# Optimization experiments

Hardware: AMD Instinct MI355X
Metric: run time of the kernel (lower is better)

The kernel has to match this reference:

```python
import jax, jax.numpy as jnp
import numpy as np

VOCAB, EMB, HID = 32000, 512, 1024
B, T = 16, 128


def setup_inputs() -> dict:
    key = jax.random.key(0)
    ks = jax.random.split(key, 12)
    bound = 1.0 / np.sqrt(HID)
    u = lambda k, shape: jax.random.uniform(k, shape, jnp.float32, -bound, bound)
    return {
        "sentence": jax.random.randint(ks[0], (B, T), 0, VOCAB),
        "emb": jax.random.normal(ks[1], (VOCAB, EMB), jnp.float32),
        "W_i": u(ks[2], (EMB + HID, HID)), "b_i": u(ks[3], (HID,)),
        "W_f": u(ks[4], (EMB + HID, HID)), "b_f": u(ks[5], (HID,)),
        "W_o": u(ks[6], (EMB + HID, HID)), "b_o": u(ks[7], (HID,)),
        "W_c": u(ks[8], (EMB + HID, HID)), "b_c": u(ks[9], (HID,)),
        "W_hq": u(ks[10], (HID, VOCAB)), "b_q": u(ks[11], (VOCAB,)),
    }


def reference(sentence, emb, W_i, b_i, W_f, b_f, W_o, b_o, W_c, b_c, W_hq, b_q):
    # [B,T,E] -> [T,B,E]
    x = jnp.swapaxes(emb[sentence], 0, 1)
    # Fuse the 4 gate matmuls into one concatenated-weight matmul (same math).
    W = jnp.concatenate([W_i, W_f, W_o, W_c], axis=1)  # [E+H, 4H]
    b = jnp.concatenate([b_i, b_f, b_o, b_c])          # [4H]
    h0 = jnp.zeros((x.shape[1], HID), x.dtype)

    def step(carry, xt):
        h, c = carry
        z = jnp.concatenate([xt, h], axis=1) @ W + b   # [B,4H]
        i, f, o, g = jnp.split(z, 4, axis=1)
        i, f, o = jax.nn.sigmoid(i), jax.nn.sigmoid(f), jax.nn.sigmoid(o)
        c = f * c + i * jnp.tanh(g)
        h = o * jnp.tanh(c)
        return (h, c), h

    _, hs = jax.lax.scan(step, (h0, h0), x)            # [T,B,H]
    out = jnp.einsum('tbh,hv->tbv', hs, W_hq) + b_q    # [T,B,V]
    return jnp.transpose(out, (1, 2, 0))               # [B,V,T] as in torch permute(1,2,0)
```

## Files before the change

kernel.cpp:

```cpp
#include <hip/hip_runtime.h>
#include <math.h>

typedef float f32x4 __attribute__((ext_vector_type(4)));
typedef short bf16x8 __attribute__((ext_vector_type(8)));
typedef unsigned short u16;
typedef unsigned int u32;

#define FLAG_STRIDE 16
#define ACQ_BASE    8192
#define EPOCH_BASE  8448
#define QCNT_BASE   8512
#define FLAG_WORDS  ((QCNT_BASE + 16) * FLAG_STRIDE)
#define NTILE       125

__device__ __forceinline__ u16 f2bf(float f) {
    union { float f; unsigned u; } x; x.f = f;
    unsigned r = x.u + 0x7fff + ((x.u >> 16) & 1);
    return (u16)(r >> 16);
}

__device__ __forceinline__ void gload_lds16(const u16* g, u16* l) {
    __builtin_amdgcn_global_load_lds(
        (const __attribute__((address_space(1))) void*)g,
        (__attribute__((address_space(3))) void*)l, 16, 0, 0);
}

__global__ __launch_bounds__(256) void prep(
    const int* __restrict__ sent, const float* __restrict__ emb, u16* __restrict__ xb,
    const float* __restrict__ bi, const float* __restrict__ bf_,
    const float* __restrict__ bo, const float* __restrict__ bc, float* __restrict__ b4,
    const float* __restrict__ Wi, const float* __restrict__ Wf,
    const float* __restrict__ Wo, const float* __restrict__ Wc, u16* __restrict__ wxt,
    const float* __restrict__ Whq, u16* __restrict__ whqt) {
    __shared__ float tile[32][33];
    const int bx = blockIdx.x, tid = threadIdx.x;
    if (bx < 1024) {
        int row = bx * 2 + (tid >> 7);
        int t = row >> 4, b = row & 15;
        int idx = sent[b * 128 + t];
        float4 v = ((const float4*)(emb + (size_t)idx * 512))[tid & 127];
        ushort4 s = { f2bf(v.x), f2bf(v.y), f2bf(v.z), f2bf(v.w) };
        ((ushort4*)(xb + (size_t)row * 512))[tid & 127] = s;
        return;
    }
    if (bx < 1040) {
        int i = (bx - 1024) * 256 + tid;
        const float* p = (i < 1024) ? bi : (i < 2048) ? bf_ : (i < 3072) ? bo : bc;
        b4[i] = p[i & 1023];
        return;
    }
    const float* in; u16* out; int ldin, ldout, rt, ct;
    if (bx < 3088) {
        int q = bx - 1040, g = q >> 9, r = q & 511;
        in = (g == 0) ? Wi : (g == 1) ? Wf : (g == 2) ? Wo : Wc;
        ldin = 1024; out = wxt + (size_t)g * 1024 * 512; ldout = 512;
        rt = (r >> 5) * 32; ct = (r & 31) * 32;
    } else {
        int q = bx - 3088;
        in = Whq; ldin = 32000; out = whqt; ldout = 1024;
        rt = (q / 1000) * 32; ct = (q % 1000) * 32;
    }
    {
        int r = tid >> 3, cq = (tid & 7) * 4;
        float4 v = *(const float4*)(in + (size_t)(rt + r) * ldin + ct + cq);
        tile[r][cq] = v.x; tile[r][cq + 1] = v.y; tile[r][cq + 2] = v.z; tile[r][cq + 3] = v.w;
        __syncthreads();
        int c = tid >> 3, rq = (tid & 7) * 4;
        ushort4 s = { f2bf(tile[rq][c]), f2bf(tile[rq + 1][c]),
                      f2bf(tile[rq + 2][c]), f2bf(tile[rq + 3][c]) };
        *(ushort4*)(out + (size_t)(ct + c) * ldout + rt + rq) = s;
    }
}

__global__ __launch_bounds__(256) void gemm_xz(
    const u16* __restrict__ A, const u16* __restrict__ Bt,
    const float* __restrict__ bias, float* __restrict__ C) {
    const int tid = threadIdx.x;
    const int l = tid & 63, w = tid >> 6;
    const int wr = w >> 1, wc = w & 1;
    const int m0 = blockIdx.x * 128, n0 = blockIdx.y * 128;
    const int K = 512;
    __shared__ __align__(16) u16 As[128 * 64];
    __shared__ __align__(16) u16 Bs[128 * 64];
    f32x4 acc[4][4];
    f32x4 zz = { 0.f, 0.f, 0.f, 0.f };
#pragma unroll
    for (int i = 0; i < 4; i++)
#pragma unroll
        for (int j = 0; j < 4; j++) acc[i][j] = zz;
    for (int kt = 0; kt < (K >> 6); ++kt) {
        __syncthreads();
#pragma unroll
        for (int i = 0; i < 4; i++) {
            int cbase = i * 256 + w * 64;
            int c = cbase + l, row = c >> 3, kc = c & 7;
            gload_lds16(A + (size_t)(m0 + row) * K + kt * 64 + kc * 8, As + (size_t)cbase * 8);
            gload_lds16(Bt + (size_t)(n0 + row) * K + kt * 64 + kc * 8, Bs + (size_t)cbase * 8);
        }
        __syncthreads();
#pragma unroll
        for (int kk = 0; kk < 2; kk++) {
            bf16x8 af[4], bfv[4];
#pragma unroll
            for (int mi = 0; mi < 4; mi++)
                af[mi] = *(const bf16x8*)(As + (wr * 64 + mi * 16 + (l & 15)) * 64 + kk * 32 + (l >> 4) * 8);
#pragma unroll
            for (int ni = 0; ni < 4; ni++)
                bfv[ni] = *(const bf16x8*)(Bs + (wc * 64 + ni * 16 + (l & 15)) * 64 + kk * 32 + (l >> 4) * 8);
#pragma unroll
            for (int mi = 0; mi < 4; mi++)
#pragma unroll
                for (int ni = 0; ni < 4; ni++)
                    acc[mi][ni] = __builtin_amdgcn_mfma_f32_16x16x32_bf16(af[mi], bfv[ni], acc[mi][ni], 0, 0, 0);
        }
    }
    const int lr = l >> 4, lc = l & 15;
#pragma unroll
    for (int ni = 0; ni < 4; ni++) {
        int col = n0 + wc * 64 + ni * 16 + lc;
        float bv = bias[col];
#pragma unroll
        for (int mi = 0; mi < 4; mi++)
#pragma unroll
            for (int r = 0; r < 4; r++) {
                int row = m0 + wr * 64 + mi * 16 + lr * 4 + r;
                C[(size_t)row * 4096 + col] = acc[mi][ni][r] + bv;
            }
    }
}

__global__ __launch_bounds__(512, 2) void lstm_proj(
    u16* __restrict__ hs,
    const float* __restrict__ xz,
    const float* __restrict__ Wi, const float* __restrict__ Wf,
    const float* __restrict__ Wo, const float* __restrict__ Wc,
    u32* __restrict__ flags,
    const u16* __restrict__ whqt,
    const float* __restrict__ bq, float* __restrict__ out) {
    __shared__ __align__(16) char smem[98816];
    const int bx = blockIdx.x;
    const int tid = threadIdx.x;
    const int w = tid >> 6, l = tid & 63;

    if (tid == 0)
        __hip_atomic_fetch_add(&flags[(size_t)(ACQ_BASE + (bx & 255)) * FLAG_STRIDE], 0u,
                               __ATOMIC_ACQ_REL, __HIP_MEMORY_SCOPE_AGENT);

    if (bx < 64) {
        u16* hstage = (u16*)smem;
        float (*zlds)[16][17] = (float (*)[16][17])(void*)(smem + 32768);
        u32* lds_cnt = (u32*)(smem + 37632);
        const int j = bx;
        const int row = l & 15, hi = l >> 4;
        if (tid == 0) *lds_cnt = 0;

        bf16x8 wf[32];
        if (w < 4) {
            const float* Wg = (w == 0) ? Wi : (w == 1) ? Wf : (w == 2) ? Wo : Wc;
#pragma unroll
            for (int kk = 0; kk < 32; ++kk)
#pragma unroll
                for (int e = 0; e < 8; ++e)
                    wf[kk][e] = f2bf(Wg[(size_t)(512 + kk * 32 + hi * 8 + e) * 1024 + j * 16 + row]);
        }
        __syncthreads();

        const int b = tid >> 4, hc = tid & 15;
        float cst = 0.f;
        float cz0 = 0.f, cz1 = 0.f, cz2 = 0.f, cz3 = 0.f;
        if (tid < 256) {
            const float* xr0 = xz + (size_t)b * 4096 + j * 16 + hc;
            cz0 = xr0[0]; cz1 = xr0[1024]; cz2 = xr0[2048]; cz3 = xr0[3072];
        }

        for (int t = 0; t < 128; ++t) {
            if (t > 0) {
                const u16* hbase = hs + (size_t)(t - 1) * 16 * 1024;
                {
                    int spins = 0;
                    while (true) {
                        u32 f = 1u;
                        if (l < 8)
                            f = __hip_atomic_load(
                                    &flags[(size_t)((t - 1) * 64 + 8 * w + l) * FLAG_STRIDE],
                                    __ATOMIC_RELAXED, __HIP_MEMORY_SCOPE_SYSTEM);
                        if (__ballot(f != 0u) == ~0ull) break;
                        __builtin_amdgcn_s_sleep(1);
                        if (++spins > (1 << 20)) break;
                    }
                }
#pragma unroll
                for (int q = 0; q < 4; ++q) {
                    int jw0 = 8 * w + 2 * q;
                    gload_lds16(hbase + (size_t)((l & 31) >> 1) * 1024
                                      + (jw0 + (l >> 5)) * 16 + (l & 1) * 8,
                                hstage + (size_t)jw0 * 256);
                }
            }
            float nz0 = 0.f, nz1 = 0.f, nz2 = 0.f, nz3 = 0.f;
            if (t < 127 && tid < 256) {
                const float* xr = xz + (size_t)((t + 1) * 16 + b) * 4096 + j * 16 + hc;
                nz0 = xr[0]; nz1 = xr[1024]; nz2 = xr[2048]; nz3 = xr[3072];
            }
            __syncthreads();
            if (t > 0) {
                if (tid == 0)
                    __hip_atomic_store(&flags[(size_t)(EPOCH_BASE + j) * FLAG_STRIDE], (u32)t,
                                       __ATOMIC_RELAXED, __HIP_MEMORY_SCOPE_SYSTEM);
                if (w < 4) {
                    f32x4 zv = { 0.f, 0.f, 0.f, 0.f };
                    f32x4 ac0 = zv, ac1 = zv, ac2 = zv, ac3 = zv;
#pragma unroll
                    for (int kk = 0; kk < 32; kk += 4) {
#pragma unroll
                        for (int u = 0; u < 4; ++u) {
                            int base = (2 * (kk + u) + (hi >> 1)) * 256 + row * 16 + (hi & 1) * 8;
                            bf16x8 a = *(const bf16x8*)(hstage + base);
                            f32x4& ac = (u == 0) ? ac0 : (u == 1) ? ac1 : (u == 2) ? ac2 : ac3;
                            ac = __builtin_amdgcn_mfma_f32_16x16x32_bf16(a, wf[kk + u], ac, 0, 0, 0);
                        }
                    }
                    f32x4 acc = (ac0 + ac1) + (ac2 + ac3);
#pragma unroll
                    for (int r = 0; r < 4; ++r)
                        zlds[w][hi * 4 + r][row] = acc[r];
                }
            }
            __syncthreads();
            if (tid < 256) {
                float zi = cz0, zf = cz1, zo = cz2, zc = cz3;
                if (t > 0) {
                    zi += zlds[0][b][hc]; zf += zlds[1][b][hc];
                    zo += zlds[2][b][hc]; zc += zlds[3][b][hc];
                }
                float ig = 1.f / (1.f + __expf(-zi));
                float fg = 1.f / (1.f + __expf(-zf));
                float og = 1.f / (1.f + __expf(-zo));
                float gg = tanhf(zc);
                cst = fg * cst + ig * gg;
                float h = og * tanhf(cst);
                float hn = __shfl_xor(h, 1);
                if (!(l & 1)) {
                    unsigned pk = (unsigned)f2bf(h) | ((unsigned)f2bf(hn) << 16);
                    u32* dst = (u32*)hs + (((size_t)(t * 16 + b) * 1024 + j * 16 + hc) >> 1);
                    __hip_atomic_store(dst, pk, __ATOMIC_RELAXED, __HIP_MEMORY_SCOPE_SYSTEM);
                }
                cz0 = nz0; cz1 = nz1; cz2 = nz2; cz3 = nz3;
            }
            if (w < 4) {
                asm volatile("s_waitcnt vmcnt(0)" ::: "memory");
                if (l == 0) {
                    u32 old = atomicAdd(lds_cnt, 1u);
                    if (old == (u32)(4 * t + 3))
                        __hip_atomic_store(&flags[(size_t)(t * 64 + j) * FLAG_STRIDE], 1u,
                                           __ATOMIC_RELAXED, __HIP_MEMORY_SCOPE_SYSTEM);
                }
            }
        }
        if (w == 0) {
            int spins = 0;
            while (true) {
                u32 f = __hip_atomic_load(&flags[(size_t)(127 * 64 + l) * FLAG_STRIDE],
                                          __ATOMIC_RELAXED, __HIP_MEMORY_SCOPE_SYSTEM);
                if (__ballot(f != 0) == ~0ull) break;
                __builtin_amdgcn_s_sleep(1);
                if (++spins > (1 << 20)) break;
            }
            if (l == 0)
                __hip_atomic_store(&flags[(size_t)(EPOCH_BASE + j) * FLAG_STRIDE], 128u,
                                   __ATOMIC_RELAXED, __HIP_MEMORY_SCOPE_SYSTEM);
        }
        return;
    }

    u16* As = (u16*)smem;
    u16* Bs = (u16*)(smem + 32768);
    u32* idx_slot = (u32*)(smem + 98304);
    const int wr = w >> 2, wc = w & 3;
    const int lr = l >> 4, lc = l & 15;

    for (int m = 0; m < 16; ++m) {
        if (w == 0) {
            const u32 need = (u32)(8 * m + 8);
            int spins = 0;
            while (__hip_atomic_load(&flags[(size_t)(EPOCH_BASE + (bx & 63)) * FLAG_STRIDE],
                                     __ATOMIC_RELAXED, __HIP_MEMORY_SCOPE_SYSTEM) < need) {
                __builtin_amdgcn_s_sleep(8);
                if (++spins > (1 << 20)) break;
            }
        }
        __syncthreads();

        while (true) {
            if (tid == 0)
                *idx_slot = __hip_atomic_fetch_add(&flags[(size_t)(QCNT_BASE + m) * FLAG_STRIDE],
                                                   1u, __ATOMIC_RELAXED, __HIP_MEMORY_SCOPE_AGENT);
            __syncthreads();
            u32 idx = *idx_slot;
            __syncthreads();
            if (idx >= NTILE) break;
            const int n0 = (int)idx * 256;

            auto STAGE = [&](int bi, int kt) {
#pragma unroll
                for (int i = 0; i < 2; ++i) {
                    int C = i * 512 + tid, r = C >> 3, c = C & 7;
                    int sc = c ^ (r & 7);
                    int arow = (8 * m + (r & 7)) * 16 + (r >> 3);
                    gload_lds16(hs + (size_t)arow * 1024 + kt * 64 + sc * 8,
                                As + (size_t)(bi * 8192 + (i * 512 + w * 64) * 8));
                }
#pragma unroll
                for (int i = 0; i < 4; ++i) {
                    int C = i * 512 + tid, r = C >> 3, c = C & 7;
                    int sc = c ^ (r & 7);
                    gload_lds16(whqt + (size_t)(n0 + r) * 1024 + kt * 64 + sc * 8,
                                Bs + (size_t)(bi * 16384 + (i * 512 + w * 64) * 8));
                }
            };

            f32x4 acc[4][4];
            f32x4 zz = { 0.f, 0.f, 0.f, 0.f };
#pragma unroll
            for (int i = 0; i < 4; i++)
#pragma unroll
                for (int jj = 0; jj < 4; jj++) acc[i][jj] = zz;

            int cur = 0;
            STAGE(0, 0);
            __syncthreads();
            for (int kt = 0; kt < 16; ++kt) {
                if (kt + 1 < 16) STAGE(cur ^ 1, kt + 1);
                const u16* Ab = As + cur * 8192;
                const u16* Bb = Bs + cur * 16384;
#pragma unroll
                for (int kk = 0; kk < 2; ++kk) {
                    bf16x8 af[4], bf[4];
#pragma unroll
                    for (int mi = 0; mi < 4; ++mi) {
                        int rA = wr * 64 + mi * 16 + lc;
                        int s = (kk * 4 + lr) ^ (rA & 7);
                        af[mi] = *(const bf16x8*)(Ab + rA * 64 + s * 8);
                    }
#pragma unroll
                    for (int ni = 0; ni < 4; ++ni) {
                        int rB = wc * 64 + ni * 16 + lc;
                        int s = (kk * 4 + lr) ^ (rB & 7);
                        bf[ni] = *(const bf16x8*)(Bb + rB * 64 + s * 8);
                    }
#pragma unroll
                    for (int mi = 0; mi < 4; ++mi)
#pragma unroll
                        for (int ni = 0; ni < 4; ++ni)
                            acc[mi][ni] = __builtin_amdgcn_mfma_f32_16x16x32_bf16(af[mi], bf[ni], acc[mi][ni], 0, 0, 0);
                }
                __syncthreads();
                cur ^= 1;
            }
#pragma unroll
            for (int ni = 0; ni < 4; ni++) {
                int col = n0 + wc * 64 + ni * 16 + lc;
                float bv = bq[col];
#pragma unroll
                for (int mi = 0; mi < 4; mi++) {
                    int r0 = wr * 64 + mi * 16 + lr * 4;
                    int bb = r0 >> 3;
                    int t0 = 8 * m + (r0 & 7);
                    float4 st = { acc[mi][ni][0] + bv, acc[mi][ni][1] + bv,
                                  acc[mi][ni][2] + bv, acc[mi][ni][3] + bv };
                    *(float4*)(out + (size_t)bb * 4096000 + (size_t)col * 128 + t0) = st;
                }
            }
        }
    }
}

extern "C" void kernel_launch(void* const* d_in, const int* in_sizes, int n_in,
                              void* d_out, int out_size, void* d_ws, size_t ws_size,
                              hipStream_t stream) {
    const int*   sent = (const int*)d_in[0];
    const float* emb  = (const float*)d_in[1];
    const float* W_i  = (const float*)d_in[2];
    const float* b_i  = (const float*)d_in[3];
    const float* W_f  = (const float*)d_in[4];
    const float* b_f  = (const float*)d_in[5];
    const float* W_o  = (const float*)d_in[6];
    const float* b_o  = (const float*)d_in[7];
    const float* W_c  = (const float*)d_in[8];
    const float* b_c  = (const float*)d_in[9];
    const float* W_hq = (const float*)d_in[10];
    const float* b_q  = (const float*)d_in[11];
    float* out = (float*)d_out;

    char* ws = (char*)d_ws;
    size_t off = 0;
    auto alloc = [&](size_t bytes) { void* p = ws + off; off += (bytes + 255) & ~255ull; return p; };
    u32*   flags = (u32*)alloc((size_t)FLAG_WORDS * 4);
    float* b4   = (float*)alloc((size_t)4096 * 4);
    u16*   xb   = (u16*)alloc((size_t)2048 * 512 * 2);
    u16*   wxt  = (u16*)alloc((size_t)4096 * 512 * 2);
    u16*   hs   = (u16*)alloc((size_t)2048 * 1024 * 2);
    float* xz   = (float*)alloc((size_t)2048 * 4096 * 4);
    u16*   whqt = (u16*)alloc((size_t)32000 * 1024 * 2);

    hipMemsetAsync(flags, 0, (size_t)FLAG_WORDS * 4, stream);
    prep<<<35088, 256, 0, stream>>>(sent, emb, xb, b_i, b_f, b_o, b_c, b4,
                                    W_i, W_f, W_o, W_c, wxt, W_hq, whqt);
    gemm_xz<<<dim3(16, 32), 256, 0, stream>>>(xb, wxt, b4, xz);
    lstm_proj<<<256, 512, 0, stream>>>(hs, xz, W_i, W_f, W_o, W_c,
                                       flags, whqt, b_q, out);
}
```

Before: 662.5 us.

## Overlap W_hq bf16 transpose with LSTM recurrence in idle projection blocks

Moves the large W_hq fp32-to-bf16 transpose out of the prep kernel and into the 192 projection blocks of the persistent lstm_proj kernel, which would otherwise sit idle while the 64 recurrence blocks step through time. A completion counter gates the first projection tile on all transposes being done. The h-state store is also widened to one 16-byte store per 8 lanes using shuffles. The risk is that the transpose traffic competes for memory bandwidth with the latency-bound recurrence.

```diff
diff --git a/kernel.cpp b/kernel.cpp
--- a/kernel.cpp
+++ b/kernel.cpp
@@ -3,14 +3,17 @@
 
 typedef float f32x4 __attribute__((ext_vector_type(4)));
 typedef short bf16x8 __attribute__((ext_vector_type(8)));
+typedef unsigned int uint4v __attribute__((ext_vector_type(4)));
 typedef unsigned short u16;
 typedef unsigned int u32;
+typedef unsigned long long u64;
 
 #define FLAG_STRIDE 16
 #define ACQ_BASE    8192
 #define EPOCH_BASE  8448
 #define QCNT_BASE   8512
-#define FLAG_WORDS  ((QCNT_BASE + 16) * FLAG_STRIDE)
+#define TCNT_BASE   8528
+#define FLAG_WORDS  ((TCNT_BASE + 1) * FLAG_STRIDE)
 #define NTILE       125
 
 __device__ __forceinline__ u16 f2bf(float f) {
@@ -30,8 +33,7 @@
     const float* __restrict__ bi, const float* __restrict__ bf_,
     const float* __restrict__ bo, const float* __restrict__ bc, float* __restrict__ b4,
     const float* __restrict__ Wi, const float* __restrict__ Wf,
-    const float* __restrict__ Wo, const float* __restrict__ Wc, u16* __restrict__ wxt,
-    const float* __restrict__ Whq, u16* __restrict__ whqt) {
+    const float* __restrict__ Wo, const float* __restrict__ Wc, u16* __restrict__ wxt) {
     __shared__ float tile[32][33];
     const int bx = blockIdx.x, tid = threadIdx.x;
     if (bx < 1024) {
@@ -49,26 +51,19 @@
         b4[i] = p[i & 1023];
         return;
     }
-    const float* in; u16* out; int ldin, ldout, rt, ct;
-    if (bx < 3088) {
-        int q = bx - 1040, g = q >> 9, r = q & 511;
-        in = (g == 0) ? Wi : (g == 1) ? Wf : (g == 2) ? Wo : Wc;
-        ldin = 1024; out = wxt + (size_t)g * 1024 * 512; ldout = 512;
-        rt = (r >> 5) * 32; ct = (r & 31) * 32;
-    } else {
-        int q = bx - 3088;
-        in = Whq; ldin = 32000; out = whqt; ldout = 1024;
-        rt = (q / 1000) * 32; ct = (q % 1000) * 32;
-    }
+    int q = bx - 1040, g = q >> 9, r = q & 511;
+    const float* in = (g == 0) ? Wi : (g == 1) ? Wf : (g == 2) ? Wo : Wc;
+    u16* out = wxt + (size_t)g * 1024 * 512;
+    int rt = (r >> 5) * 32, ct = (r & 31) * 32;
     {
-        int r = tid >> 3, cq = (tid & 7) * 4;
-        float4 v = *(const float4*)(in + (size_t)(rt + r) * ldin + ct + cq);
-        tile[r][cq] = v.x; tile[r][cq + 1] = v.y; tile[r][cq + 2] = v.z; tile[r][cq + 3] = v.w;
+        int rr = tid >> 3, cq = (tid & 7) * 4;
+        float4 v = *(const float4*)(in + (size_t)(rt + rr) * 1024 + ct + cq);
+        tile[rr][cq] = v.x; tile[rr][cq + 1] = v.y; tile[rr][cq + 2] = v.z; tile[rr][cq + 3] = v.w;
         __syncthreads();
         int c = tid >> 3, rq = (tid & 7) * 4;
         ushort4 s = { f2bf(tile[rq][c]), f2bf(tile[rq + 1][c]),
                       f2bf(tile[rq + 2][c]), f2bf(tile[rq + 3][c]) };
-        *(ushort4*)(out + (size_t)(ct + c) * ldout + rt + rq) = s;
+        *(ushort4*)(out + (size_t)(ct + c) * 512 + rt + rq) = s;
     }
 }
 
@@ -135,7 +130,8 @@
     const float* __restrict__ Wi, const float* __restrict__ Wf,
     const float* __restrict__ Wo, const float* __restrict__ Wc,
     u32* __restrict__ flags,
-    const u16* __restrict__ whqt,
+    const float* __restrict__ Whq,
+    u16* __restrict__ whqt,
     const float* __restrict__ bq, float* __restrict__ out) {
     __shared__ __align__(16) char smem[98816];
     const int bx = blockIdx.x;
@@ -240,10 +236,15 @@
                 cst = fg * cst + ig * gg;
                 float h = og * tanhf(cst);
                 float hn = __shfl_xor(h, 1);
-                if (!(l & 1)) {
-                    unsigned pk = (unsigned)f2bf(h) | ((unsigned)f2bf(hn) << 16);
-                    u32* dst = (u32*)hs + (((size_t)(t * 16 + b) * 1024 + j * 16 + hc) >> 1);
-                    __hip_atomic_store(dst, pk, __ATOMIC_RELAXED, __HIP_MEMORY_SCOPE_SYSTEM);
+                u32 pk0 = (u32)f2bf(h) | ((u32)f2bf(hn) << 16);
+                u32 p2  = __shfl_xor(pk0, 2);
+                u32 p4a = __shfl_xor(pk0, 4);
+                u32 p4b = __shfl_xor(p2, 4);
+                if (!(l & 7)) {
+                    uint4v v = { pk0, p2, p4a, p4b };
+                    u16* dst = hs + (size_t)(t * 16 + b) * 1024 + j * 16 + hc;
+                    asm volatile("global_store_dwordx4 %0, %1, off sc0 sc1"
+                                 :: "v"(dst), "v"(v) : "memory");
                 }
                 cz0 = nz0; cz1 = nz1; cz2 = nz2; cz3 = nz3;
             }
@@ -273,6 +274,38 @@
         return;
     }
 
+    {
+        float (*tp)[32][33] = (float (*)[32][33])(void*)smem;
+        const int half = tid >> 8, t256 = tid & 255;
+        const int r = t256 >> 3, cq = (t256 & 7) * 4;
+        const int c = t256 >> 3, rq = (t256 & 7) * 4;
+        for (int it = 0; it < 84; ++it) {
+            int q = it * 384 + (bx - 64) * 2 + half;
+            bool act = q < 32000;
+            int rt = 0, ct = 0;
+            if (act) { rt = (q / 1000) * 32; ct = (q % 1000) * 32; }
+            if (act) {
+                float4 v = *(const float4*)(Whq + (size_t)(rt + r) * 32000 + ct + cq);
+                tp[half][r][cq] = v.x; tp[half][r][cq + 1] = v.y;
+                tp[half][r][cq + 2] = v.z; tp[half][r][cq + 3] = v.w;
+            }
+            __syncthreads();
+            if (act) {
+                u64 pk = (u64)f2bf(tp[half][rq][c])
+                       | ((u64)f2bf(tp[half][rq + 1][c]) << 16)
+                       | ((u64)f2bf(tp[half][rq + 2][c]) << 32)
+                       | ((u64)f2bf(tp[half][rq + 3][c]) << 48);
+                __hip_atomic_store((u64*)(whqt + (size_t)(ct + c) * 1024 + rt + rq), pk,
+                                   __ATOMIC_RELAXED, __HIP_MEMORY_SCOPE_SYSTEM);
+            }
+            __syncthreads();
+        }
+        asm volatile("s_waitcnt vmcnt(0)" ::: "memory");
+        if (tid == 0)
+            __hip_atomic_fetch_add(&flags[(size_t)TCNT_BASE * FLAG_STRIDE], 1u,
+                                   __ATOMIC_RELAXED, __HIP_MEMORY_SCOPE_SYSTEM);
+    }
+
     u16* As = (u16*)smem;
     u16* Bs = (u16*)(smem + 32768);
     u32* idx_slot = (u32*)(smem + 98304);
@@ -283,8 +316,14 @@
         if (w == 0) {
             const u32 need = (u32)(8 * m + 8);
             int spins = 0;
-            while (__hip_atomic_load(&flags[(size_t)(EPOCH_BASE + (bx & 63)) * FLAG_STRIDE],
-                                     __ATOMIC_RELAXED, __HIP_MEMORY_SCOPE_SYSTEM) < need) {
+            while (true) {
+                u32 e = __hip_atomic_load(&flags[(size_t)(EPOCH_BASE + (bx & 63)) * FLAG_STRIDE],
+                                          __ATOMIC_RELAXED, __HIP_MEMORY_SCOPE_SYSTEM);
+                u32 tc = 192u;
+                if (m == 0)
+                    tc = __hip_atomic_load(&flags[(size_t)TCNT_BASE * FLAG_STRIDE],
+                                           __ATOMIC_RELAXED, __HIP_MEMORY_SCOPE_SYSTEM);
+                if (e >= need && tc >= 192u) break;
                 __builtin_amdgcn_s_sleep(8);
                 if (++spins > (1 << 20)) break;
             }
@@ -404,9 +443,9 @@
     u16*   whqt = (u16*)alloc((size_t)32000 * 1024 * 2);
 
     hipMemsetAsync(flags, 0, (size_t)FLAG_WORDS * 4, stream);
-    prep<<<35088, 256, 0, stream>>>(sent, emb, xb, b_i, b_f, b_o, b_c, b4,
-                                    W_i, W_f, W_o, W_c, wxt, W_hq, whqt);
+    prep<<<3088, 256, 0, stream>>>(sent, emb, xb, b_i, b_f, b_o, b_c, b4,
+                                   W_i, W_f, W_o, W_c, wxt);
     gemm_xz<<<dim3(16, 32), 256, 0, stream>>>(xb, wxt, b4, xz);
     lstm_proj<<<256, 512, 0, stream>>>(hs, xz, W_i, W_f, W_o, W_c,
-                                       flags, whqt, b_q, out);
-}
+                                       flags, W_hq, whqt, b_q, out);
+}
```

Result: no change. 666.8 us (+0.7%).

## Halve LSTM recurrence blocks to 32 with two waves per gate

Applied to the files above, without the earlier changes.

The recurrent LSTM phase now runs on 32 blocks instead of 64. Each block owns 32 hidden columns, and all 8 waves do MFMA work, two per gate. This cuts the number of per-step flags each block polls and shrinks the cross-block barrier fan-in. The h staging uses an XOR-swizzled LDS layout, and h stores are packed into 16-byte dwordx4 writes instead of dword atomics. Each block now does twice the gate and elementwise work per step, and more blocks are left for the projection GEMM.

```diff
diff --git a/kernel.cpp b/kernel.cpp
--- a/kernel.cpp
+++ b/kernel.cpp
@@ -3,8 +3,10 @@
 
 typedef float f32x4 __attribute__((ext_vector_type(4)));
 typedef short bf16x8 __attribute__((ext_vector_type(8)));
+typedef unsigned int uint4v __attribute__((ext_vector_type(4)));
 typedef unsigned short u16;
 typedef unsigned int u32;
+typedef unsigned long long u64;
 
 #define FLAG_STRIDE 16
 #define ACQ_BASE    8192
@@ -12,6 +14,7 @@
 #define QCNT_BASE   8512
 #define FLAG_WORDS  ((QCNT_BASE + 16) * FLAG_STRIDE)
 #define NTILE       125
+#define NLSTM       32
 
 __device__ __forceinline__ u16 f2bf(float f) {
     union { float f; unsigned u; } x; x.f = f;
@@ -146,32 +149,29 @@
         __hip_atomic_fetch_add(&flags[(size_t)(ACQ_BASE + (bx & 255)) * FLAG_STRIDE], 0u,
                                __ATOMIC_ACQ_REL, __HIP_MEMORY_SCOPE_AGENT);
 
-    if (bx < 64) {
+    if (bx < NLSTM) {
         u16* hstage = (u16*)smem;
-        float (*zlds)[16][17] = (float (*)[16][17])(void*)(smem + 32768);
-        u32* lds_cnt = (u32*)(smem + 37632);
+        float (*zlds)[16][33] = (float (*)[16][33])(void*)(smem + 32768);
+        u32* lds_cnt = (u32*)(smem + 41472);
         const int j = bx;
         const int row = l & 15, hi = l >> 4;
+        const int g = w >> 1, ch = w & 1;
         if (tid == 0) *lds_cnt = 0;
 
+        const float* Wg = (g == 0) ? Wi : (g == 1) ? Wf : (g == 2) ? Wo : Wc;
         bf16x8 wf[32];
-        if (w < 4) {
-            const float* Wg = (w == 0) ? Wi : (w == 1) ? Wf : (w == 2) ? Wo : Wc;
-#pragma unroll
-            for (int kk = 0; kk < 32; ++kk)
-#pragma unroll
-                for (int e = 0; e < 8; ++e)
-                    wf[kk][e] = f2bf(Wg[(size_t)(512 + kk * 32 + hi * 8 + e) * 1024 + j * 16 + row]);
-        }
+#pragma unroll
+        for (int kk = 0; kk < 32; ++kk)
+#pragma unroll
+            for (int e = 0; e < 8; ++e)
+                wf[kk][e] = f2bf(Wg[(size_t)(512 + kk * 32 + hi * 8 + e) * 1024
+                                    + j * 32 + ch * 16 + row]);
         __syncthreads();
 
-        const int b = tid >> 4, hc = tid & 15;
+        const int b = tid >> 5, hc = tid & 31;
         float cst = 0.f;
-        float cz0 = 0.f, cz1 = 0.f, cz2 = 0.f, cz3 = 0.f;
-        if (tid < 256) {
-            const float* xr0 = xz + (size_t)b * 4096 + j * 16 + hc;
-            cz0 = xr0[0]; cz1 = xr0[1024]; cz2 = xr0[2048]; cz3 = xr0[3072];
-        }
+        const float* xr0 = xz + (size_t)b * 4096 + j * 32 + hc;
+        float cz0 = xr0[0], cz1 = xr0[1024], cz2 = xr0[2048], cz3 = xr0[3072];
 
         for (int t = 0; t < 128; ++t) {
             if (t > 0) {
@@ -180,9 +180,9 @@
                     int spins = 0;
                     while (true) {
                         u32 f = 1u;
-                        if (l < 8)
+                        if (l < 4)
                             f = __hip_atomic_load(
-                                    &flags[(size_t)((t - 1) * 64 + 8 * w + l) * FLAG_STRIDE],
+                                    &flags[(size_t)((t - 1) * 32 + 4 * w + l) * FLAG_STRIDE],
                                     __ATOMIC_RELAXED, __HIP_MEMORY_SCOPE_SYSTEM);
                         if (__ballot(f != 0u) == ~0ull) break;
                         __builtin_amdgcn_s_sleep(1);
@@ -191,15 +191,15 @@
                 }
 #pragma unroll
                 for (int q = 0; q < 4; ++q) {
-                    int jw0 = 8 * w + 2 * q;
-                    gload_lds16(hbase + (size_t)((l & 31) >> 1) * 1024
-                                      + (jw0 + (l >> 5)) * 16 + (l & 1) * 8,
-                                hstage + (size_t)jw0 * 256);
+                    int js = 4 * w + q;
+                    int sr = l >> 2, sub = l & 3;
+                    gload_lds16(hbase + (size_t)sr * 1024 + js * 32 + (sub ^ (sr & 3)) * 8,
+                                hstage + (size_t)js * 512);
                 }
             }
             float nz0 = 0.f, nz1 = 0.f, nz2 = 0.f, nz3 = 0.f;
-            if (t < 127 && tid < 256) {
-                const float* xr = xz + (size_t)((t + 1) * 16 + b) * 4096 + j * 16 + hc;
+            if (t < 127) {
+                const float* xr = xz + (size_t)((t + 1) * 16 + b) * 4096 + j * 32 + hc;
                 nz0 = xr[0]; nz1 = xr[1024]; nz2 = xr[2048]; nz3 = xr[3072];
             }
             __syncthreads();
@@ -207,27 +207,26 @@
                 if (tid == 0)
                     __hip_atomic_store(&flags[(size_t)(EPOCH_BASE + j) * FLAG_STRIDE], (u32)t,
                                        __ATOMIC_RELAXED, __HIP_MEMORY_SCOPE_SYSTEM);
-                if (w < 4) {
-                    f32x4 zv = { 0.f, 0.f, 0.f, 0.f };
-                    f32x4 ac0 = zv, ac1 = zv, ac2 = zv, ac3 = zv;
-#pragma unroll
-                    for (int kk = 0; kk < 32; kk += 4) {
-#pragma unroll
-                        for (int u = 0; u < 4; ++u) {
-                            int base = (2 * (kk + u) + (hi >> 1)) * 256 + row * 16 + (hi & 1) * 8;
-                            bf16x8 a = *(const bf16x8*)(hstage + base);
-                            f32x4& ac = (u == 0) ? ac0 : (u == 1) ? ac1 : (u == 2) ? ac2 : ac3;
-                            ac = __builtin_amdgcn_mfma_f32_16x16x32_bf16(a, wf[kk + u], ac, 0, 0, 0);
-                        }
+                f32x4 zv = { 0.f, 0.f, 0.f, 0.f };
+                f32x4 ac0 = zv, ac1 = zv, ac2 = zv, ac3 = zv;
+#pragma unroll
+                for (int kk = 0; kk < 32; kk += 4) {
+#pragma unroll
+                    for (int u = 0; u < 4; ++u) {
+                        int c = kk + u;
+                        bf16x8 a = *(const bf16x8*)(hstage + c * 512 + row * 32
+                                                    + (hi ^ (row & 3)) * 8);
+                        f32x4& ac = (u == 0) ? ac0 : (u == 1) ? ac1 : (u == 2) ? ac2 : ac3;
+                        ac = __builtin_amdgcn_mfma_f32_16x16x32_bf16(a, wf[c], ac, 0, 0, 0);
                     }
-                    f32x4 acc = (ac0 + ac1) + (ac2 + ac3);
-#pragma unroll
-                    for (int r = 0; r < 4; ++r)
-                        zlds[w][hi * 4 + r][row] = acc[r];
-                }
+                }
+                f32x4 acc = (ac0 + ac1) + (ac2 + ac3);
+#pragma unroll
+                for (int r = 0; r < 4; ++r)
+                    zlds[g][hi * 4 + r][ch * 16 + row] = acc[r];
             }
             __syncthreads();
-            if (tid < 256) {
+            {
                 float zi = cz0, zf = cz1, zo = cz2, zc = cz3;
                 if (t > 0) {
                     zi += zlds[0][b][hc]; zf += zlds[1][b][hc];
@@ -240,27 +239,32 @@
                 cst = fg * cst + ig * gg;
                 float h = og * tanhf(cst);
                 float hn = __shfl_xor(h, 1);
-                if (!(l & 1)) {
-                    unsigned pk = (unsigned)f2bf(h) | ((unsigned)f2bf(hn) << 16);
-                    u32* dst = (u32*)hs + (((size_t)(t * 16 + b) * 1024 + j * 16 + hc) >> 1);
-                    __hip_atomic_store(dst, pk, __ATOMIC_RELAXED, __HIP_MEMORY_SCOPE_SYSTEM);
+                u32 pk0 = (u32)f2bf(h) | ((u32)f2bf(hn) << 16);
+                u32 p2  = __shfl_xor(pk0, 2);
+                u32 p4a = __shfl_xor(pk0, 4);
+                u32 p4b = __shfl_xor(p2, 4);
+                if (!(l & 7)) {
+                    uint4v v = { pk0, p2, p4a, p4b };
+                    u16* dst = hs + (size_t)(t * 16 + b) * 1024 + j * 32 + hc;
+                    asm volatile("global_store_dwordx4 %0, %1, off sc0 sc1"
+                                 :: "v"(dst), "v"(v) : "memory");
                 }
                 cz0 = nz0; cz1 = nz1; cz2 = nz2; cz3 = nz3;
             }
-            if (w < 4) {
-                asm volatile("s_waitcnt vmcnt(0)" ::: "memory");
-                if (l == 0) {
-                    u32 old = atomicAdd(lds_cnt, 1u);
-                    if (old == (u32)(4 * t + 3))
-                        __hip_atomic_store(&flags[(size_t)(t * 64 + j) * FLAG_STRIDE], 1u,
-                                           __ATOMIC_RELAXED, __HIP_MEMORY_SCOPE_SYSTEM);
-                }
+            asm volatile("s_waitcnt vmcnt(0)" ::: "memory");
+            if (l == 0) {
+                u32 old = atomicAdd(lds_cnt, 1u);
+                if (old == (u32)(8 * t + 7))
+                    __hip_atomic_store(&flags[(size_t)(t * 32 + j) * FLAG_STRIDE], 1u,
+                                       __ATOMIC_RELAXED, __HIP_MEMORY_SCOPE_SYSTEM);
             }
         }
         if (w == 0) {
             int spins = 0;
             while (true) {
-                u32 f = __hip_atomic_load(&flags[(size_t)(127 * 64 + l) * FLAG_STRIDE],
+                u32 f = 1u;
+                if (l < 32)
+                    f = __hip_atomic_load(&flags[(size_t)(127 * 32 + l) * FLAG_STRIDE],
                                           __ATOMIC_RELAXED, __HIP_MEMORY_SCOPE_SYSTEM);
                 if (__ballot(f != 0) == ~0ull) break;
                 __builtin_amdgcn_s_sleep(1);
@@ -283,7 +287,7 @@
         if (w == 0) {
             const u32 need = (u32)(8 * m + 8);
             int spins = 0;
-            while (__hip_atomic_load(&flags[(size_t)(EPOCH_BASE + (bx & 63)) * FLAG_STRIDE],
+            while (__hip_atomic_load(&flags[(size_t)(EPOCH_BASE + (bx & 31)) * FLAG_STRIDE],
                                      __ATOMIC_RELAXED, __HIP_MEMORY_SCOPE_SYSTEM) < need) {
                 __builtin_amdgcn_s_sleep(8);
                 if (++spins > (1 << 20)) break;
```

New measurement: 730.3 us. 1.1x slower.
